# Kernel tuning notes

Measured on AMD Instinct MI355X. Metric: run time of the kernel, lower is better.

The kernel has to match this reference:

```python
import jax, jax.numpy as jnp
import numpy as np

EPS = 1e-7  # K.epsilon()
ROUTINGS = 3

def squash(v, axis=-1):
    s2 = jnp.sum(jnp.square(v), axis=axis, keepdims=True)
    scale = s2 / (1.0 + s2) / jnp.sqrt(s2 + EPS)
    return scale * v

def setup_inputs() -> dict:
    key = jax.random.key(0)
    k1, k2 = jax.random.split(key)
    B, N, I = 128, 512, 256   # batch, input_num_capsule, input_dim_capsule
    M, D = 32, 16             # num_capsule, dim_capsule
    x = jax.random.normal(k1, (B, N, I), dtype=jnp.float32)
    W = jax.random.normal(k2, (M, N, D, I), dtype=jnp.float32) * 0.05
    return {"x": x, "W": W}

def reference(x, W):
    # x: [B,N,I], W: [M,N,D,I]
    # inputs_hat[b,m,n,d] = sum_i x[b,n,i] * W[m,n,d,i]
    inputs_hat = jnp.einsum('bni,mndi->bmnd', x, W)
    B, M, N, _ = inputs_hat.shape
    b = jnp.zeros((B, M, N), dtype=inputs_hat.dtype)
    outputs = None
    for i in range(ROUTINGS):
        c = jax.nn.softmax(b, axis=1)  # softmax over num_capsule dim (dim=1)
        s = jnp.einsum('bmn,bmnd->bmd', c, inputs_hat)
        outputs = squash(s)
        if i < ROUTINGS - 1:
            b = b + jnp.einsum('bmd,bmnd->bmn', outputs, inputs_hat)
    return outputs
```

## Files before the change

### kernel.cpp

```cpp
#include <hip/hip_runtime.h>
#include <stdint.h>

#define B_ 128
#define N_ 512
#define I_ 256
#define M_ 32
#define D_ 16

typedef __attribute__((ext_vector_type(4))) float f32x4;
typedef __attribute__((ext_vector_type(4))) float float4v;
typedef __attribute__((ext_vector_type(8))) short short8;
typedef __attribute__((ext_vector_type(4))) unsigned int u32x4;
typedef __attribute__((ext_vector_type(4))) unsigned short ushort4v;

__device__ __forceinline__ float bf2f(unsigned short u) {
    union { unsigned int i; float f; } v; v.i = ((unsigned int)u) << 16; return v.f;
}
__device__ __forceinline__ unsigned short f2bf(float f) {
    union { float f; unsigned int i; } v; v.f = f;
    unsigned int r = v.i + 0x7FFFu + ((v.i >> 16) & 1u);
    return (unsigned short)(r >> 16);
}

__device__ __forceinline__ void gload16(const void* g, void* l) {
    __builtin_amdgcn_global_load_lds(
        (const __attribute__((address_space(1))) void*)g,
        (__attribute__((address_space(3))) void*)l, 16, 0, 0);
}

__global__ __launch_bounds__(256) void conv_x(const float* __restrict__ x,
                                              unsigned short* __restrict__ xT) {
    const int rid = blockIdx.x * 4 + (threadIdx.x >> 6);
    const int i0  = (threadIdx.x & 63) * 4;
    const int b   = rid >> 9;
    const int n   = rid & 511;
    float4v v = *(const float4v*)(x + (size_t)rid * I_ + i0);
    ushort4v h;
    h[0] = f2bf(v[0]); h[1] = f2bf(v[1]); h[2] = f2bf(v[2]); h[3] = f2bf(v[3]);
    *(ushort4v*)(xT + ((size_t)(n * B_ + b)) * I_ + i0) = h;
}

__device__ __forceinline__ short8 ldfragB(const float* rowp, int r15, int g0) {
    const f32x4* rp = (const f32x4*)rowp;
    f32x4 lo = rp[g0 ^ r15];
    f32x4 hi = rp[(g0 + 1) ^ r15];
    unsigned int u0, u1, u2, u3;
    asm("v_cvt_pk_bf16_f32 %0, %1, %2" : "=v"(u0) : "v"(lo[0]), "v"(lo[1]));
    asm("v_cvt_pk_bf16_f32 %0, %1, %2" : "=v"(u1) : "v"(lo[2]), "v"(lo[3]));
    asm("v_cvt_pk_bf16_f32 %0, %1, %2" : "=v"(u2) : "v"(hi[0]), "v"(hi[1]));
    asm("v_cvt_pk_bf16_f32 %0, %1, %2" : "=v"(u3) : "v"(hi[2]), "v"(hi[3]));
    u32x4 uv = {u0, u1, u2, u3};
    return __builtin_bit_cast(short8, uv);
}

__global__ __launch_bounds__(256) void hat_gemm(const float* __restrict__ W,
                                                const unsigned short* __restrict__ xT,
                                                unsigned short* __restrict__ hat) {
    __shared__ float Bs[64][256];

    const int n    = blockIdx.y;
    const int mc   = blockIdx.x;
    const int tid  = threadIdx.x;
    const int lane = tid & 63;
    const int w    = tid >> 6;
    const int l15  = lane & 15;

    {
        const size_t mbase = (((size_t)(mc * 4 + w) * N_ + n) * D_) * I_;
        #pragma unroll
        for (int j = 0; j < 16; ++j) {
            const float* src = W + mbase + (size_t)j * I_ + ((lane ^ j) << 2);
            gload16(src, &Bs[w * 16 + j][0]);
        }
    }

    const unsigned short* xrow0 = xT + ((size_t)(n * B_) + w * 32 + l15) * I_;
    auto loadA = [&](int a, int ks) -> short8 {
        return *(const short8*)(xrow0 + (size_t)a * 16 * I_ + ks * 32 + (lane >> 4) * 8);
    };

    short8 pa0[4], pa1[4];
    #pragma unroll
    for (int j = 0; j < 4; ++j) { pa0[j] = loadA(0, j); pa1[j] = loadA(1, j); }

    f32x4 acc[2][4];
    #pragma unroll
    for (int a = 0; a < 2; ++a)
        #pragma unroll
        for (int c = 0; c < 4; ++c) { f32x4 z = {0.f, 0.f, 0.f, 0.f}; acc[a][c] = z; }

    __syncthreads();

    #pragma unroll
    for (int ks = 0; ks < 8; ++ks) {
        short8 a0 = pa0[ks & 3];
        short8 a1 = pa1[ks & 3];
        if (ks < 4) { pa0[ks & 3] = loadA(0, ks + 4); pa1[ks & 3] = loadA(1, ks + 4); }
        const int g0 = ks * 8 + (lane >> 4) * 2;
        #pragma unroll
        for (int ct = 0; ct < 4; ++ct) {
            short8 bb = ldfragB(&Bs[ct * 16 + l15][0], l15, g0);
            acc[0][ct] = __builtin_amdgcn_mfma_f32_16x16x32_bf16(a0, bb, acc[0][ct], 0, 0, 0);
            acc[1][ct] = __builtin_amdgcn_mfma_f32_16x16x32_bf16(a1, bb, acc[1][ct], 0, 0, 0);
        }
    }

    const int d  = l15;
    const int rq = lane >> 4;
    #pragma unroll
    for (int rt = 0; rt < 2; ++rt) {
        #pragma unroll
        for (int ct = 0; ct < 4; ++ct) {
            const int m = mc * 4 + ct;
            #pragma unroll
            for (int r = 0; r < 4; ++r) {
                const int brow = w * 32 + rt * 16 + rq * 4 + r;
                const size_t idx = (((size_t)brow * M_ + m) * N_ + n) * D_ + d;
                hat[idx] = f2bf(acc[rt][ct][r]);
            }
        }
    }
}

__global__ __launch_bounds__(512) void routing(const unsigned short* __restrict__ hat,
                                               float* __restrict__ out) {
    __shared__ float blog[M_][N_];
    __shared__ float cmax[N_];
    __shared__ float rcsum[N_];

    const int b    = blockIdx.x;
    const int tid  = threadIdx.x;
    const int lane = tid & 63;
    const int w    = tid >> 6;

    #pragma unroll
    for (int m = 0; m < M_; ++m) blog[m][tid] = 0.f;
    __syncthreads();

    float ov[4][16];

    for (int it = 0; it < 3; ++it) {
        {
            float mx = -3.4e38f;
            #pragma unroll
            for (int m = 0; m < M_; ++m) mx = fmaxf(mx, blog[m][tid]);
            float s = 0.f;
            #pragma unroll
            for (int m = 0; m < M_; ++m) s += __expf(blog[m][tid] - mx);
            cmax[tid]  = mx;
            rcsum[tid] = 1.f / s;
        }
        __syncthreads();

        float sacc[4][16];
        #pragma unroll
        for (int q = 0; q < 4; ++q)
            #pragma unroll
            for (int dd = 0; dd < 16; ++dd) sacc[q][dd] = 0.f;

        for (int r = 0; r < 8; ++r) {
            const int nn = r * 64 + lane;
            #pragma unroll
            for (int q = 0; q < 4; ++q) {
                const int m = w * 4 + q;
                const float cm = __expf(blog[m][nn] - cmax[nn]) * rcsum[nn];
                const size_t base = (((size_t)b * M_ + m) * N_ + nn) * D_;
                short8 h0 = *(const short8*)(hat + base);
                short8 h1 = *(const short8*)(hat + base + 8);
                #pragma unroll
                for (int dd = 0; dd < 8; ++dd) {
                    sacc[q][dd]     += cm * bf2f((unsigned short)h0[dd]);
                    sacc[q][8 + dd] += cm * bf2f((unsigned short)h1[dd]);
                }
            }
        }
        #pragma unroll
        for (int off = 32; off >= 1; off >>= 1) {
            #pragma unroll
            for (int q = 0; q < 4; ++q)
                #pragma unroll
                for (int dd = 0; dd < 16; ++dd)
                    sacc[q][dd] += __shfl_xor(sacc[q][dd], off, 64);
        }
        #pragma unroll
        for (int q = 0; q < 4; ++q) {
            float s2 = 0.f;
            #pragma unroll
            for (int dd = 0; dd < 16; ++dd) s2 += sacc[q][dd] * sacc[q][dd];
            const float scale = s2 / (1.f + s2) / sqrtf(s2 + 1e-7f);
            #pragma unroll
            for (int dd = 0; dd < 16; ++dd) ov[q][dd] = scale * sacc[q][dd];
        }

        if (it < 2) {
            for (int r = 0; r < 8; ++r) {
                const int nn = r * 64 + lane;
                #pragma unroll
                for (int q = 0; q < 4; ++q) {
                    const int m = w * 4 + q;
                    const size_t base = (((size_t)b * M_ + m) * N_ + nn) * D_;
                    short8 h0 = *(const short8*)(hat + base);
                    short8 h1 = *(const short8*)(hat + base + 8);
                    float dot = 0.f;
                    #pragma unroll
                    for (int dd = 0; dd < 8; ++dd) {
                        dot += ov[q][dd]     * bf2f((unsigned short)h0[dd]);
                        dot += ov[q][8 + dd] * bf2f((unsigned short)h1[dd]);
                    }
                    blog[m][nn] += dot;
                }
            }
        }
        __syncthreads();
    }

    if (lane == 0) {
        #pragma unroll
        for (int q = 0; q < 4; ++q) {
            const int m = w * 4 + q;
            #pragma unroll
            for (int c4 = 0; c4 < 4; ++c4) {
                float4v v;
                v[0] = ov[q][c4 * 4 + 0];
                v[1] = ov[q][c4 * 4 + 1];
                v[2] = ov[q][c4 * 4 + 2];
                v[3] = ov[q][c4 * 4 + 3];
                *(float4v*)&out[((size_t)b * M_ + m) * D_ + c4 * 4] = v;
            }
        }
    }
}

extern "C" void kernel_launch(void* const* d_in, const int* in_sizes, int n_in,
                              void* d_out, int out_size, void* d_ws, size_t ws_size,
                              hipStream_t stream) {
    const float* x = (const float*)d_in[0];
    const float* W = (const float*)d_in[1];
    unsigned short* hat = (unsigned short*)d_ws;
    unsigned short* xT  = (unsigned short*)((char*)d_ws + (size_t)64 * 1024 * 1024);
    float* out = (float*)d_out;

    conv_x<<<dim3((B_ * N_) / 4), dim3(256), 0, stream>>>(x, xT);
    hat_gemm<<<dim3(8, N_), dim3(256), 0, stream>>>(W, xT, hat);
    routing<<<dim3(B_), dim3(512), 0, stream>>>(hat, out);
}
```

Before: 197.4 us.

## Restructure hat GEMM to one wave per (m,n) reading W directly into registers

Replaces the 256-thread block that staged a 64x256 fp32 W tile in LDS with single-wave blocks, one per (m,n) pair. Each wave loads its W slice straight from global memory into registers, converts it to bf16, and runs the MFMA over all 128 batch rows with register double-buffering. Blocks are ordered so that consecutive blocks share m, which changes which data sits in cache together. This removes the LDS staging and barrier, but each wave now re-reads the xT tile for its n from global or cache, 32 times per n instead of 8.

```diff
diff --git a/kernel.cpp b/kernel.cpp
--- a/kernel.cpp
+++ b/kernel.cpp
@@ -22,10 +22,14 @@
     return (unsigned short)(r >> 16);
 }
 
-__device__ __forceinline__ void gload16(const void* g, void* l) {
-    __builtin_amdgcn_global_load_lds(
-        (const __attribute__((address_space(1))) void*)g,
-        (__attribute__((address_space(3))) void*)l, 16, 0, 0);
+__device__ __forceinline__ short8 cvt8(float4v lo, float4v hi) {
+    unsigned int u0, u1, u2, u3;
+    asm("v_cvt_pk_bf16_f32 %0, %1, %2" : "=v"(u0) : "v"(lo[0]), "v"(lo[1]));
+    asm("v_cvt_pk_bf16_f32 %0, %1, %2" : "=v"(u1) : "v"(lo[2]), "v"(lo[3]));
+    asm("v_cvt_pk_bf16_f32 %0, %1, %2" : "=v"(u2) : "v"(hi[0]), "v"(hi[1]));
+    asm("v_cvt_pk_bf16_f32 %0, %1, %2" : "=v"(u3) : "v"(hi[2]), "v"(hi[3]));
+    u32x4 uv = {u0, u1, u2, u3};
+    return __builtin_bit_cast(short8, uv);
 }
 
 __global__ __launch_bounds__(256) void conv_x(const float* __restrict__ x,
@@ -40,84 +44,61 @@
     *(ushort4v*)(xT + ((size_t)(n * B_ + b)) * I_ + i0) = h;
 }
 
-__device__ __forceinline__ short8 ldfragB(const float* rowp, int r15, int g0) {
-    const f32x4* rp = (const f32x4*)rowp;
-    f32x4 lo = rp[g0 ^ r15];
-    f32x4 hi = rp[(g0 + 1) ^ r15];
-    unsigned int u0, u1, u2, u3;
-    asm("v_cvt_pk_bf16_f32 %0, %1, %2" : "=v"(u0) : "v"(lo[0]), "v"(lo[1]));
-    asm("v_cvt_pk_bf16_f32 %0, %1, %2" : "=v"(u1) : "v"(lo[2]), "v"(lo[3]));
-    asm("v_cvt_pk_bf16_f32 %0, %1, %2" : "=v"(u2) : "v"(hi[0]), "v"(hi[1]));
-    asm("v_cvt_pk_bf16_f32 %0, %1, %2" : "=v"(u3) : "v"(hi[2]), "v"(hi[3]));
-    u32x4 uv = {u0, u1, u2, u3};
-    return __builtin_bit_cast(short8, uv);
-}
-
-__global__ __launch_bounds__(256) void hat_gemm(const float* __restrict__ W,
-                                                const unsigned short* __restrict__ xT,
-                                                unsigned short* __restrict__ hat) {
-    __shared__ float Bs[64][256];
-
-    const int n    = blockIdx.y;
-    const int mc   = blockIdx.x;
-    const int tid  = threadIdx.x;
-    const int lane = tid & 63;
-    const int w    = tid >> 6;
+__global__ __launch_bounds__(64) void hat_gemm(const float* __restrict__ W,
+                                               const unsigned short* __restrict__ xT,
+                                               unsigned short* __restrict__ hat) {
+    const int L   = blockIdx.x;
+    const int t   = (L & 7) * 2048 + (L >> 3);
+    const int n   = t >> 5;
+    const int m   = t & 31;
+
+    const int lane = threadIdx.x;
     const int l15  = lane & 15;
-
-    {
-        const size_t mbase = (((size_t)(mc * 4 + w) * N_ + n) * D_) * I_;
-        #pragma unroll
-        for (int j = 0; j < 16; ++j) {
-            const float* src = W + mbase + (size_t)j * I_ + ((lane ^ j) << 2);
-            gload16(src, &Bs[w * 16 + j][0]);
-        }
-    }
-
-    const unsigned short* xrow0 = xT + ((size_t)(n * B_) + w * 32 + l15) * I_;
-    auto loadA = [&](int a, int ks) -> short8 {
-        return *(const short8*)(xrow0 + (size_t)a * 16 * I_ + ks * 32 + (lane >> 4) * 8);
-    };
-
-    short8 pa0[4], pa1[4];
-    #pragma unroll
-    for (int j = 0; j < 4; ++j) { pa0[j] = loadA(0, j); pa1[j] = loadA(1, j); }
-
-    f32x4 acc[2][4];
-    #pragma unroll
-    for (int a = 0; a < 2; ++a)
-        #pragma unroll
-        for (int c = 0; c < 4; ++c) { f32x4 z = {0.f, 0.f, 0.f, 0.f}; acc[a][c] = z; }
-
-    __syncthreads();
+    const int kq   = lane >> 4;
+
+    const unsigned short* abase = xT + ((size_t)n * B_ + l15) * I_ + kq * 8;
+    const float* wbase = W + (((size_t)m * N_ + n) * D_ + l15) * I_ + kq * 8;
+
+    f32x4 acc[8];
+    #pragma unroll
+    for (int a = 0; a < 8; ++a) { f32x4 z = {0.f, 0.f, 0.f, 0.f}; acc[a] = z; }
+
+    short8 acur[8], anxt[8];
+    float4v blo, bhi, nlo, nhi;
+
+    #pragma unroll
+    for (int a = 0; a < 8; ++a)
+        acur[a] = *(const short8*)(abase + (size_t)a * 16 * I_);
+    blo = *(const float4v*)(wbase);
+    bhi = *(const float4v*)(wbase + 4);
 
     #pragma unroll
     for (int ks = 0; ks < 8; ++ks) {
-        short8 a0 = pa0[ks & 3];
-        short8 a1 = pa1[ks & 3];
-        if (ks < 4) { pa0[ks & 3] = loadA(0, ks + 4); pa1[ks & 3] = loadA(1, ks + 4); }
-        const int g0 = ks * 8 + (lane >> 4) * 2;
-        #pragma unroll
-        for (int ct = 0; ct < 4; ++ct) {
-            short8 bb = ldfragB(&Bs[ct * 16 + l15][0], l15, g0);
-            acc[0][ct] = __builtin_amdgcn_mfma_f32_16x16x32_bf16(a0, bb, acc[0][ct], 0, 0, 0);
-            acc[1][ct] = __builtin_amdgcn_mfma_f32_16x16x32_bf16(a1, bb, acc[1][ct], 0, 0, 0);
-        }
-    }
-
-    const int d  = l15;
-    const int rq = lane >> 4;
-    #pragma unroll
-    for (int rt = 0; rt < 2; ++rt) {
-        #pragma unroll
-        for (int ct = 0; ct < 4; ++ct) {
-            const int m = mc * 4 + ct;
-            #pragma unroll
-            for (int r = 0; r < 4; ++r) {
-                const int brow = w * 32 + rt * 16 + rq * 4 + r;
-                const size_t idx = (((size_t)brow * M_ + m) * N_ + n) * D_ + d;
-                hat[idx] = f2bf(acc[rt][ct][r]);
-            }
+        if (ks < 7) {
+            #pragma unroll
+            for (int a = 0; a < 8; ++a)
+                anxt[a] = *(const short8*)(abase + (size_t)a * 16 * I_ + (ks + 1) * 32);
+            nlo = *(const float4v*)(wbase + (ks + 1) * 32);
+            nhi = *(const float4v*)(wbase + (ks + 1) * 32 + 4);
+        }
+        short8 bb = cvt8(blo, bhi);
+        #pragma unroll
+        for (int a = 0; a < 8; ++a)
+            acc[a] = __builtin_amdgcn_mfma_f32_16x16x32_bf16(acur[a], bb, acc[a], 0, 0, 0);
+        if (ks < 7) {
+            #pragma unroll
+            for (int a = 0; a < 8; ++a) acur[a] = anxt[a];
+            blo = nlo; bhi = nhi;
+        }
+    }
+
+    #pragma unroll
+    for (int a = 0; a < 8; ++a) {
+        #pragma unroll
+        for (int r = 0; r < 4; ++r) {
+            const int brow = a * 16 + kq * 4 + r;
+            const size_t idx = (((size_t)brow * M_ + m) * N_ + n) * D_ + l15;
+            hat[idx] = f2bf(acc[a][r]);
         }
     }
 }
@@ -241,6 +222,6 @@
     float* out = (float*)d_out;
 
     conv_x<<<dim3((B_ * N_) / 4), dim3(256), 0, stream>>>(x, xT);
-    hat_gemm<<<dim3(8, N_), dim3(256), 0, stream>>>(W, xT, hat);
+    hat_gemm<<<dim3(M_ * N_), dim3(64), 0, stream>>>(W, xT, hat);
     routing<<<dim3(B_), dim3(512), 0, stream>>>(hat, out);
 }
```

After: 296.1 us. +50.0%, slower.
